# Kernel optimization log

Hardware: AMD Instinct MI355X
Metric: run time of the kernel (lower is better)

Reference implementation:

```python
import jax, jax.numpy as jnp
import numpy as np

B, S, D_IN, D_HID, D_OUT = 8, 2048, 1024, 1024, 1024


def setup_inputs() -> dict:
    key = jax.random.key(0)
    ks = jax.random.split(key, 11)
    def lin(kw, kb, fan_in, fan_out):
        bound = 1.0 / np.sqrt(fan_in)
        W = jax.random.uniform(kw, (fan_out, fan_in), minval=-bound, maxval=bound, dtype=jnp.float32)
        b = jax.random.uniform(kb, (fan_out,), minval=-bound, maxval=bound, dtype=jnp.float32)
        return W, b
    Wq, bq = lin(ks[0], ks[1], D_IN, D_HID)
    Wk, bk = lin(ks[2], ks[3], D_IN, D_HID)
    Wv, bv = lin(ks[4], ks[5], D_IN, D_HID)
    Wo, bo = lin(ks[6], ks[7], D_HID, D_OUT)
    gamma = jnp.ones((D_OUT,), jnp.float32)
    beta = jnp.zeros((D_OUT,), jnp.float32)
    x = jax.random.normal(ks[8], (B, S, D_IN), dtype=jnp.float32)
    return {"x": x, "Wq": Wq, "bq": bq, "Wk": Wk, "bk": bk,
            "Wv": Wv, "bv": bv, "Wo": Wo, "bo": bo,
            "gamma": gamma, "beta": beta}


def _layer_norm(x, gamma, beta, eps=1e-5):
    mu = jnp.mean(x, axis=-1, keepdims=True)
    var = jnp.var(x, axis=-1, keepdims=True)
    return (x - mu) * jax.lax.rsqrt(var + eps) * gamma + beta


def reference(x, Wq, bq, Wk, bk, Wv, bv, Wo, bo, gamma, beta):
    q = jnp.einsum('bsd,hd->bsh', x, Wq) + bq   # [B,S,H]
    k = jnp.einsum('bsd,hd->bsh', x, Wk) + bk
    v = jnp.einsum('bsd,hd->bsh', x, Wv) + bv
    scale = 1.0 / jnp.sqrt(jnp.float32(D_HID))
    scores = jnp.einsum('bqh,bkh->bqk', q, k) * scale  # [B,S,S]
    attn = jax.nn.softmax(scores, axis=-1)
    weighted = jnp.einsum('bqk,bkh->bqh', attn, v)     # [B,S,H]
    out = jnp.einsum('bsh,oh->bso', weighted, Wo) + bo # [B,S,O]
    return _layer_norm(out + x, gamma, beta)
```

## Files before the change

### kernel.cpp

```cpp
#include <hip/hip_runtime.h>
#include <hip/hip_bf16.h>
#include <math.h>


typedef __bf16 bf16;
typedef unsigned char u8;
typedef __attribute__((ext_vector_type(8))) __bf16 bf16x8;
typedef __attribute__((ext_vector_type(4))) __bf16 bf16x4;
typedef __attribute__((ext_vector_type(8))) int i32x8;
typedef __attribute__((ext_vector_type(16))) float f32x16;

__device__ __forceinline__ void async16(const u8* g, u8* l) {
    __builtin_amdgcn_global_load_lds(
        (const __attribute__((address_space(1))) void*)g,
        (__attribute__((address_space(3))) void*)l, 16, 0, 0);
}

#define WAITCNT_VM(n) __builtin_amdgcn_s_waitcnt((15 << 8) | (7 << 4) | (n))

__device__ __forceinline__ u8 to_fp8(float v) {
    return (u8)(__builtin_amdgcn_cvt_pk_fp8_f32(v, v, 0, 0) & 0xFF);
}

__global__ __launch_bounds__(256) void cast_f32_fp8(
    const float* __restrict__ in, u8* __restrict__ out, int n)
{
    int i = (blockIdx.x * 256 + threadIdx.x) * 8;
    if (i >= n) return;
    float4 a = *(const float4*)(in + i);
    float4 b = *(const float4*)(in + i + 4);
    int lo = __builtin_amdgcn_cvt_pk_fp8_f32(a.x, a.y, 0, 0);
    lo = __builtin_amdgcn_cvt_pk_fp8_f32(a.z, a.w, lo, 1);
    int hi = __builtin_amdgcn_cvt_pk_fp8_f32(b.x, b.y, 0, 0);
    hi = __builtin_amdgcn_cvt_pk_fp8_f32(b.z, b.w, hi, 1);
    int2 o = { lo, hi };
    *(int2*)(out + i) = o;
}

__global__ __launch_bounds__(256) void gemm_f8(
    const u8* __restrict__ A, long lda, long sA,
    const u8* __restrict__ B, long ldb, long sB,
    void* __restrict__ Cv, long ldc, long sC,
    const float* __restrict__ bias, int bias_mode,
    float scale, int c_mode, int K)
{
    __shared__ u8 lds[3][16384];

    const int gx = gridDim.x, gy = gridDim.y;
    const int slice = gx * gy;
    const int total = slice * gridDim.z;
    int flat = ((int)blockIdx.z * gy + (int)blockIdx.y) * gx + (int)blockIdx.x;
    if ((total & 7) == 0)
        flat = (flat & 7) * (total >> 3) + (flat >> 3);
    const int bz = flat / slice;
    const int rem = flat - bz * slice;
    const int by = rem / gx;
    const int bx = rem - by * gx;

    const int tid = threadIdx.x;
    const long tM = (long)by * 128;
    const long tN = (long)bx * 128;
    A += (long)bz * sA;
    B += (long)bz * sB;

    const int ra = tid >> 2;
    const int posc = tid & 3;
    const int ca = (posc ^ (ra & 3)) * 16;
    const u8* ga0 = A + (tM + ra) * lda + ca;
    const u8* ga1 = ga0 + 64 * lda;
    const u8* gb0 = B + (tN + ra) * ldb + ca;
    const u8* gb1 = gb0 + 64 * ldb;
    const int lo0 = tid * 16;
    const int lo1 = 4096 + tid * 16;
    const int lo2 = 8192 + tid * 16;
    const int lo3 = 12288 + tid * 16;

    const int w = tid >> 6, lane = tid & 63;
    const int wm = (w & 1) * 64, wn = (w >> 1) * 64;
    const int r32 = lane & 31, kh = lane >> 5;

    f32x16 acc[2][2] = {};

    const int iters = K >> 6;

    {
        u8* p0 = lds[0];
        async16(ga0, p0 + lo0); async16(ga1, p0 + lo1);
        async16(gb0, p0 + lo2); async16(gb1, p0 + lo3);
        u8* p1 = lds[1];
        async16(ga0 + 64, p1 + lo0); async16(ga1 + 64, p1 + lo1);
        async16(gb0 + 64, p1 + lo2); async16(gb1 + 64, p1 + lo3);
    }

    const int rowA0 = wm + r32, rowA1 = wm + 32 + r32;
    const int rowB0 = wn + r32, rowB1 = wn + 32 + r32;
    const int c0 = kh * 2, c1 = kh * 2 + 1;
    const int offA0q0 = rowA0 * 64 + ((c0 ^ (rowA0 & 3)) << 4);
    const int offA0q1 = rowA0 * 64 + ((c1 ^ (rowA0 & 3)) << 4);
    const int offA1q0 = rowA1 * 64 + ((c0 ^ (rowA1 & 3)) << 4);
    const int offA1q1 = rowA1 * 64 + ((c1 ^ (rowA1 & 3)) << 4);
    const int offB0q0 = 8192 + rowB0 * 64 + ((c0 ^ (rowB0 & 3)) << 4);
    const int offB0q1 = 8192 + rowB0 * 64 + ((c1 ^ (rowB0 & 3)) << 4);
    const int offB1q0 = 8192 + rowB1 * 64 + ((c0 ^ (rowB1 & 3)) << 4);
    const int offB1q1 = 8192 + rowB1 * 64 + ((c1 ^ (rowB1 & 3)) << 4);

    int cur = 0;
    for (int it = 0; it < iters; ++it) {
        if (it + 1 < iters) WAITCNT_VM(4);
        else WAITCNT_VM(0);
        __builtin_amdgcn_s_barrier();

        if (it + 2 < iters) {
            int nb = cur + 2; if (nb >= 3) nb -= 3;
            u8* p = lds[nb];
            const long ko = (long)(it + 2) << 6;
            async16(ga0 + ko, p + lo0); async16(ga1 + ko, p + lo1);
            async16(gb0 + ko, p + lo2); async16(gb1 + ko, p + lo3);
        }

        const u8* curb = lds[cur];
        union F { i32x8 v; int4 q[2]; };
        F a0, a1, b0, b1;
        a0.q[0] = *(const int4*)&curb[offA0q0];
        a0.q[1] = *(const int4*)&curb[offA0q1];
        a1.q[0] = *(const int4*)&curb[offA1q0];
        a1.q[1] = *(const int4*)&curb[offA1q1];
        b0.q[0] = *(const int4*)&curb[offB0q0];
        b0.q[1] = *(const int4*)&curb[offB0q1];
        b1.q[0] = *(const int4*)&curb[offB1q0];
        b1.q[1] = *(const int4*)&curb[offB1q1];

        acc[0][0] = __builtin_amdgcn_mfma_scale_f32_32x32x64_f8f6f4(
            a0.v, b0.v, acc[0][0], 0, 0, 0, 0x7F7F7F7F, 0, 0x7F7F7F7F);
        acc[0][1] = __builtin_amdgcn_mfma_scale_f32_32x32x64_f8f6f4(
            a0.v, b1.v, acc[0][1], 0, 0, 0, 0x7F7F7F7F, 0, 0x7F7F7F7F);
        acc[1][0] = __builtin_amdgcn_mfma_scale_f32_32x32x64_f8f6f4(
            a1.v, b0.v, acc[1][0], 0, 0, 0, 0x7F7F7F7F, 0, 0x7F7F7F7F);
        acc[1][1] = __builtin_amdgcn_mfma_scale_f32_32x32x64_f8f6f4(
            a1.v, b1.v, acc[1][1], 0, 0, 0, 0x7F7F7F7F, 0, 0x7F7F7F7F);

        if (++cur >= 3) cur = 0;
    }

#pragma unroll
    for (int i = 0; i < 2; i++) {
#pragma unroll
        for (int j = 0; j < 2; j++) {
            const long gn = tN + wn + j * 32 + r32;
            const float bn = (bias_mode == 1) ? bias[gn] : 0.0f;
#pragma unroll
            for (int reg = 0; reg < 16; reg++) {
                const int rowf = (reg & 3) + 8 * (reg >> 2) + 4 * kh;
                const long gm = tM + wm + i * 32 + rowf;
                float v = acc[i][j][reg] * scale + bn;
                if (bias_mode == 2) v += bias[gm];
                if (c_mode == 0)
                    ((bf16*)Cv + (long)bz * sC)[gm * ldc + gn] = (bf16)v;
                else
                    ((u8*)Cv + (long)bz * sC)[gm * ldc + gn] = to_fp8(v);
            }
        }
    }
}

__global__ __launch_bounds__(256) void softmax_f8(
    const bf16* __restrict__ S, u8* __restrict__ P)
{
    const long row = blockIdx.x;
    const bf16* p = S + row * 2048;
    const int t = threadIdx.x;

    bf16x8 v = *(const bf16x8*)(p + t * 8);
    float f[8];
    float m = -3.0e38f;
#pragma unroll
    for (int i = 0; i < 8; i++) { f[i] = (float)v[i]; m = fmaxf(m, f[i]); }
    for (int o = 32; o; o >>= 1) m = fmaxf(m, __shfl_down(m, o));

    __shared__ float sm[4], ssum[4];
    if ((t & 63) == 0) sm[t >> 6] = m;
    __syncthreads();
    m = fmaxf(fmaxf(sm[0], sm[1]), fmaxf(sm[2], sm[3]));

    float s = 0.0f;
#pragma unroll
    for (int i = 0; i < 8; i++) { f[i] = __expf(f[i] - m); s += f[i]; }
    for (int o = 32; o; o >>= 1) s += __shfl_down(s, o);
    if ((t & 63) == 0) ssum[t >> 6] = s;
    __syncthreads();
    s = ssum[0] + ssum[1] + ssum[2] + ssum[3];

    const float c = 256.0f / s;
    int lo = __builtin_amdgcn_cvt_pk_fp8_f32(f[0] * c, f[1] * c, 0, 0);
    lo = __builtin_amdgcn_cvt_pk_fp8_f32(f[2] * c, f[3] * c, lo, 1);
    int hi = __builtin_amdgcn_cvt_pk_fp8_f32(f[4] * c, f[5] * c, 0, 0);
    hi = __builtin_amdgcn_cvt_pk_fp8_f32(f[6] * c, f[7] * c, hi, 1);
    int2 o = { lo, hi };
    *(int2*)(P + row * 2048 + t * 8) = o;
}

__global__ __launch_bounds__(256) void ln_res(
    const bf16* __restrict__ pre, const float* __restrict__ x,
    const float* __restrict__ gamma, const float* __restrict__ beta,
    float* __restrict__ out)
{
    const long row = blockIdx.x;
    const int t = threadIdx.x;
    const long base = row * 1024 + t * 4;

    bf16x4 a = *(const bf16x4*)(pre + base);
    float4 b = *(const float4*)(x + base);
    float v0 = (float)a[0] + b.x, v1 = (float)a[1] + b.y;
    float v2 = (float)a[2] + b.z, v3 = (float)a[3] + b.w;

    float s = v0 + v1 + v2 + v3;
    float q = v0 * v0 + v1 * v1 + v2 * v2 + v3 * v3;
    for (int o = 32; o; o >>= 1) { s += __shfl_down(s, o); q += __shfl_down(q, o); }

    __shared__ float ls[4], lq[4];
    if ((t & 63) == 0) { ls[t >> 6] = s; lq[t >> 6] = q; }
    __syncthreads();
    s = ls[0] + ls[1] + ls[2] + ls[3];
    q = lq[0] + lq[1] + lq[2] + lq[3];

    const float mean = s * (1.0f / 1024.0f);
    const float var = q * (1.0f / 1024.0f) - mean * mean;
    const float rstd = rsqrtf(var + 1e-5f);

    const int c = t * 4;
    float4 g = *(const float4*)(gamma + c);
    float4 be = *(const float4*)(beta + c);
    float4 o;
    o.x = (v0 - mean) * rstd * g.x + be.x;
    o.y = (v1 - mean) * rstd * g.y + be.y;
    o.z = (v2 - mean) * rstd * g.z + be.z;
    o.w = (v3 - mean) * rstd * g.w + be.w;
    *(float4*)(out + base) = o;
}

extern "C" void kernel_launch(void* const* d_in, const int* in_sizes, int n_in,
                              void* d_out, int out_size, void* d_ws, size_t ws_size,
                              hipStream_t stream)
{
    const float* x     = (const float*)d_in[0];
    const float* Wq    = (const float*)d_in[1];
    const float* bq    = (const float*)d_in[2];
    const float* Wk    = (const float*)d_in[3];
    const float* bk    = (const float*)d_in[4];
    const float* Wv    = (const float*)d_in[5];
    const float* bv    = (const float*)d_in[6];
    const float* Wo    = (const float*)d_in[7];
    const float* bo    = (const float*)d_in[8];
    const float* gamma = (const float*)d_in[9];
    const float* beta  = (const float*)d_in[10];
    float* out = (float*)d_out;

    char* ws = (char*)d_ws;
    u8* x8  = (u8*)(ws + (size_t)0);
    u8* Q8  = (u8*)(ws + (size_t)16777216);
    u8* K8  = (u8*)(ws + (size_t)33554432);
    u8* VT8 = (u8*)(ws + (size_t)50331648);
    u8* P8  = (u8*)(ws + (size_t)67108864);
    bf16* Sb = (bf16*)(ws + (size_t)104857600);
    u8* Wq8 = (u8*)(ws + (size_t)176160768);
    u8* Wk8 = Wq8 + 1048576;
    u8* Wv8 = Wk8 + 1048576;
    u8* Wo8 = Wv8 + 1048576;

    cast_f32_fp8<<<8192, 256, 0, stream>>>(x, x8, 16777216);
    cast_f32_fp8<<<512, 256, 0, stream>>>(Wq, Wq8, 1048576);
    cast_f32_fp8<<<512, 256, 0, stream>>>(Wk, Wk8, 1048576);
    cast_f32_fp8<<<512, 256, 0, stream>>>(Wv, Wv8, 1048576);
    cast_f32_fp8<<<512, 256, 0, stream>>>(Wo, Wo8, 1048576);

    gemm_f8<<<dim3(8, 128, 1), 256, 0, stream>>>(
        x8, 1024, 0, Wq8, 1024, 0, (void*)Q8, 1024, 0, bq, 1, 1.0f, 1, 1024);
    gemm_f8<<<dim3(8, 128, 1), 256, 0, stream>>>(
        x8, 1024, 0, Wk8, 1024, 0, (void*)K8, 1024, 0, bk, 1, 1.0f, 1, 1024);
    gemm_f8<<<dim3(128, 8, 1), 256, 0, stream>>>(
        Wv8, 1024, 0, x8, 1024, 0, (void*)VT8, 16384, 0, bv, 2, 1.0f, 1, 1024);
    gemm_f8<<<dim3(16, 16, 8), 256, 0, stream>>>(
        Q8, 1024, 2097152, K8, 1024, 2097152, (void*)Sb, 2048, 4194304,
        nullptr, 0, 0.03125f, 0, 1024);
    softmax_f8<<<16384, 256, 0, stream>>>(Sb, P8);
    gemm_f8<<<dim3(8, 16, 8), 256, 0, stream>>>(
        P8, 2048, 4194304, VT8, 16384, 2048, (void*)Q8, 1024, 2097152,
        nullptr, 0, 0.0625f, 1, 2048);
    gemm_f8<<<dim3(8, 128, 1), 256, 0, stream>>>(
        Q8, 1024, 0, Wo8, 1024, 0, (void*)Sb, 1024, 0, bo, 1, 0.0625f, 0, 1024);
    ln_res<<<16384, 256, 0, stream>>>((const bf16*)Sb, x, gamma, beta, out);
}
```

Baseline: 454.3 us.

## Double the FP8 GEMM K-tile to 128 with double-buffered LDS

The FP8 MFMA GEMM now loads 128-wide K tiles into two 32 KB LDS buffers with an 8-chunk XOR swizzle, replacing the three-deep ring of 64-wide tiles. Each iteration issues 8 async loads and 8 MFMAs, which halves the number of barriers and loop iterations. In exchange, prefetch depth drops from two tiles ahead to one, and the loop waits for all outstanding loads (waitcnt 0) every iteration. LDS per block grows from 48 KB to 64 KB, which may reduce occupancy.

```diff
diff --git a/kernel.cpp b/kernel.cpp
--- a/kernel.cpp
+++ b/kernel.cpp
@@ -44,7 +44,7 @@
     const float* __restrict__ bias, int bias_mode,
     float scale, int c_mode, int K)
 {
-    __shared__ u8 lds[3][16384];
+    __shared__ u8 lds[2][32768];
 
     const int gx = gridDim.x, gy = gridDim.y;
     const int slice = gx * gy;
@@ -63,17 +63,11 @@
     A += (long)bz * sA;
     B += (long)bz * sB;
 
-    const int ra = tid >> 2;
-    const int posc = tid & 3;
-    const int ca = (posc ^ (ra & 3)) * 16;
-    const u8* ga0 = A + (tM + ra) * lda + ca;
-    const u8* ga1 = ga0 + 64 * lda;
-    const u8* gb0 = B + (tN + ra) * ldb + ca;
-    const u8* gb1 = gb0 + 64 * ldb;
-    const int lo0 = tid * 16;
-    const int lo1 = 4096 + tid * 16;
-    const int lo2 = 8192 + tid * 16;
-    const int lo3 = 12288 + tid * 16;
+    const int srow = tid >> 3;
+    const int schunk = (tid & 7) ^ (srow & 7);
+    const u8* gAs = A + (tM + srow) * lda + schunk * 16;
+    const u8* gBs = B + (tN + srow) * ldb + schunk * 16;
+    const int ldst = tid * 16;
 
     const int w = tid >> 6, lane = tid & 63;
     const int wm = (w & 1) * 64, wn = (w >> 1) * 64;
@@ -81,65 +75,86 @@
 
     f32x16 acc[2][2] = {};
 
-    const int iters = K >> 6;
+    const int iters = K >> 7;
 
     {
-        u8* p0 = lds[0];
-        async16(ga0, p0 + lo0); async16(ga1, p0 + lo1);
-        async16(gb0, p0 + lo2); async16(gb1, p0 + lo3);
-        u8* p1 = lds[1];
-        async16(ga0 + 64, p1 + lo0); async16(ga1 + 64, p1 + lo1);
-        async16(gb0 + 64, p1 + lo2); async16(gb1 + 64, p1 + lo3);
+        u8* p = lds[0];
+        async16(gAs,            p + ldst);
+        async16(gAs + 32 * lda, p + 4096 + ldst);
+        async16(gAs + 64 * lda, p + 8192 + ldst);
+        async16(gAs + 96 * lda, p + 12288 + ldst);
+        async16(gBs,            p + 16384 + ldst);
+        async16(gBs + 32 * ldb, p + 20480 + ldst);
+        async16(gBs + 64 * ldb, p + 24576 + ldst);
+        async16(gBs + 96 * ldb, p + 28672 + ldst);
     }
 
-    const int rowA0 = wm + r32, rowA1 = wm + 32 + r32;
-    const int rowB0 = wn + r32, rowB1 = wn + 32 + r32;
-    const int c0 = kh * 2, c1 = kh * 2 + 1;
-    const int offA0q0 = rowA0 * 64 + ((c0 ^ (rowA0 & 3)) << 4);
-    const int offA0q1 = rowA0 * 64 + ((c1 ^ (rowA0 & 3)) << 4);
-    const int offA1q0 = rowA1 * 64 + ((c0 ^ (rowA1 & 3)) << 4);
-    const int offA1q1 = rowA1 * 64 + ((c1 ^ (rowA1 & 3)) << 4);
-    const int offB0q0 = 8192 + rowB0 * 64 + ((c0 ^ (rowB0 & 3)) << 4);
-    const int offB0q1 = 8192 + rowB0 * 64 + ((c1 ^ (rowB0 & 3)) << 4);
-    const int offB1q0 = 8192 + rowB1 * 64 + ((c0 ^ (rowB1 & 3)) << 4);
-    const int offB1q1 = 8192 + rowB1 * 64 + ((c1 ^ (rowB1 & 3)) << 4);
+    const int xr = r32 & 7;
+    const int rA0 = (wm + r32) * 128;
+    const int rA1 = rA0 + 32 * 128;
+    const int rB0 = 16384 + (wn + r32) * 128;
+    const int rB1 = rB0 + 32 * 128;
+    const int c00 = (((kh << 1) + 0) ^ xr) << 4;
+    const int c01 = (((kh << 1) + 1) ^ xr) << 4;
+    const int c10 = ((4 + (kh << 1) + 0) ^ xr) << 4;
+    const int c11 = ((4 + (kh << 1) + 1) ^ xr) << 4;
 
     int cur = 0;
     for (int it = 0; it < iters; ++it) {
-        if (it + 1 < iters) WAITCNT_VM(4);
-        else WAITCNT_VM(0);
+        WAITCNT_VM(0);
         __builtin_amdgcn_s_barrier();
 
-        if (it + 2 < iters) {
-            int nb = cur + 2; if (nb >= 3) nb -= 3;
-            u8* p = lds[nb];
-            const long ko = (long)(it + 2) << 6;
-            async16(ga0 + ko, p + lo0); async16(ga1 + ko, p + lo1);
-            async16(gb0 + ko, p + lo2); async16(gb1 + ko, p + lo3);
+        if (it + 1 < iters) {
+            u8* p = lds[cur ^ 1];
+            const long ko = (long)(it + 1) << 7;
+            async16(gAs + ko,            p + ldst);
+            async16(gAs + 32 * lda + ko, p + 4096 + ldst);
+            async16(gAs + 64 * lda + ko, p + 8192 + ldst);
+            async16(gAs + 96 * lda + ko, p + 12288 + ldst);
+            async16(gBs + ko,            p + 16384 + ldst);
+            async16(gBs + 32 * ldb + ko, p + 20480 + ldst);
+            async16(gBs + 64 * ldb + ko, p + 24576 + ldst);
+            async16(gBs + 96 * ldb + ko, p + 28672 + ldst);
         }
 
         const u8* curb = lds[cur];
         union F { i32x8 v; int4 q[2]; };
-        F a0, a1, b0, b1;
-        a0.q[0] = *(const int4*)&curb[offA0q0];
-        a0.q[1] = *(const int4*)&curb[offA0q1];
-        a1.q[0] = *(const int4*)&curb[offA1q0];
-        a1.q[1] = *(const int4*)&curb[offA1q1];
-        b0.q[0] = *(const int4*)&curb[offB0q0];
-        b0.q[1] = *(const int4*)&curb[offB0q1];
-        b1.q[0] = *(const int4*)&curb[offB1q0];
-        b1.q[1] = *(const int4*)&curb[offB1q1];
+        F a0k0, a1k0, b0k0, b1k0, a0k1, a1k1, b0k1, b1k1;
+        a0k0.q[0] = *(const int4*)&curb[rA0 + c00];
+        a0k0.q[1] = *(const int4*)&curb[rA0 + c01];
+        a1k0.q[0] = *(const int4*)&curb[rA1 + c00];
+        a1k0.q[1] = *(const int4*)&curb[rA1 + c01];
+        b0k0.q[0] = *(const int4*)&curb[rB0 + c00];
+        b0k0.q[1] = *(const int4*)&curb[rB0 + c01];
+        b1k0.q[0] = *(const int4*)&curb[rB1 + c00];
+        b1k0.q[1] = *(const int4*)&curb[rB1 + c01];
+        a0k1.q[0] = *(const int4*)&curb[rA0 + c10];
+        a0k1.q[1] = *(const int4*)&curb[rA0 + c11];
+        a1k1.q[0] = *(const int4*)&curb[rA1 + c10];
+        a1k1.q[1] = *(const int4*)&curb[rA1 + c11];
+        b0k1.q[0] = *(const int4*)&curb[rB0 + c10];
+        b0k1.q[1] = *(const int4*)&curb[rB0 + c11];
+        b1k1.q[0] = *(const int4*)&curb[rB1 + c10];
+        b1k1.q[1] = *(const int4*)&curb[rB1 + c11];
 
         acc[0][0] = __builtin_amdgcn_mfma_scale_f32_32x32x64_f8f6f4(
-            a0.v, b0.v, acc[0][0], 0, 0, 0, 0x7F7F7F7F, 0, 0x7F7F7F7F);
+            a0k0.v, b0k0.v, acc[0][0], 0, 0, 0, 0x7F7F7F7F, 0, 0x7F7F7F7F);
         acc[0][1] = __builtin_amdgcn_mfma_scale_f32_32x32x64_f8f6f4(
-            a0.v, b1.v, acc[0][1], 0, 0, 0, 0x7F7F7F7F, 0, 0x7F7F7F7F);
+            a0k0.v, b1k0.v, acc[0][1], 0, 0, 0, 0x7F7F7F7F, 0, 0x7F7F7F7F);
         acc[1][0] = __builtin_amdgcn_mfma_scale_f32_32x32x64_f8f6f4(
-            a1.v, b0.v, acc[1][0], 0, 0, 0, 0x7F7F7F7F, 0, 0x7F7F7F7F);
+            a1k0.v, b0k0.v, acc[1][0], 0, 0, 0, 0x7F7F7F7F, 0, 0x7F7F7F7F);
         acc[1][1] = __builtin_amdgcn_mfma_scale_f32_32x32x64_f8f6f4(
-            a1.v, b1.v, acc[1][1], 0, 0, 0, 0x7F7F7F7F, 0, 0x7F7F7F7F);
-
-        if (++cur >= 3) cur = 0;
+            a1k0.v, b1k0.v, acc[1][1], 0, 0, 0, 0x7F7F7F7F, 0, 0x7F7F7F7F);
+        acc[0][0] = __builtin_amdgcn_mfma_scale_f32_32x32x64_f8f6f4(
+            a0k1.v, b0k1.v, acc[0][0], 0, 0, 0, 0x7F7F7F7F, 0, 0x7F7F7F7F);
+        acc[0][1] = __builtin_amdgcn_mfma_scale_f32_32x32x64_f8f6f4(
+            a0k1.v, b1k1.v, acc[0][1], 0, 0, 0, 0x7F7F7F7F, 0, 0x7F7F7F7F);
+        acc[1][0] = __builtin_amdgcn_mfma_scale_f32_32x32x64_f8f6f4(
+            a1k1.v, b0k1.v, acc[1][0], 0, 0, 0, 0x7F7F7F7F, 0, 0x7F7F7F7F);
+        acc[1][1] = __builtin_amdgcn_mfma_scale_f32_32x32x64_f8f6f4(
+            a1k1.v, b1k1.v, acc[1][1], 0, 0, 0, 0x7F7F7F7F, 0, 0x7F7F7F7F);
+
+        cur ^= 1;
     }
 
 #pragma unroll
```

New measurement: 408.2 us. 10.2% less time.

## Use 4-stage LDS ring with issue-before-barrier prefetch and new swizzle layout

Applied to the files above, without the earlier changes.

The fp8 GEMM now keeps four LDS stages instead of three, which lets the next prefetch be issued before the wait and barrier instead of after. The shared-memory tile layout changes to 128-byte lines with an 8-way XOR swizzle, simplifying the fragment offsets. MFMA sections are wrapped in s_setprio to favor matrix issue. The intent is better overlap of global loads with compute and fewer LDS bank conflicts, at the cost of 16KB more LDS per block, which may reduce occupancy.

```diff
diff --git a/kernel.cpp b/kernel.cpp
--- a/kernel.cpp
+++ b/kernel.cpp
@@ -44,7 +44,7 @@
     const float* __restrict__ bias, int bias_mode,
     float scale, int c_mode, int K)
 {
-    __shared__ u8 lds[3][16384];
+    __shared__ u8 lds[4][16384];
 
     const int gx = gridDim.x, gy = gridDim.y;
     const int slice = gx * gy;
@@ -63,17 +63,16 @@
     A += (long)bz * sA;
     B += (long)bz * sB;
 
-    const int ra = tid >> 2;
-    const int posc = tid & 3;
-    const int ca = (posc ^ (ra & 3)) * 16;
-    const u8* ga0 = A + (tM + ra) * lda + ca;
-    const u8* ga1 = ga0 + 64 * lda;
-    const u8* gb0 = B + (tN + ra) * ldb + ca;
-    const u8* gb1 = gb0 + 64 * ldb;
-    const int lo0 = tid * 16;
-    const int lo1 = 4096 + tid * 16;
-    const int lo2 = 8192 + tid * 16;
-    const int lo3 = 12288 + tid * 16;
+    const int sline = tid >> 3;
+    const int sch = (tid & 7) ^ (sline & 7);
+    const int skb = (sch & 3) << 4;
+    const int srofs = (sch & 4) << 4;
+    const u8* gA0 = A + (tM + sline + srofs) * lda + skb;
+    const u8* gA1 = gA0 + 32 * lda;
+    const u8* gB0 = B + (tN + sline + srofs) * ldb + skb;
+    const u8* gB1 = gB0 + 32 * ldb;
+    const int dA0 = tid * 16,        dA1 = 4096 + tid * 16;
+    const int dB0 = 8192 + tid * 16, dB1 = 12288 + tid * 16;
 
     const int w = tid >> 6, lane = tid & 63;
     const int wm = (w & 1) * 64, wn = (w >> 1) * 64;
@@ -84,52 +83,49 @@
     const int iters = K >> 6;
 
     {
-        u8* p0 = lds[0];
-        async16(ga0, p0 + lo0); async16(ga1, p0 + lo1);
-        async16(gb0, p0 + lo2); async16(gb1, p0 + lo3);
-        u8* p1 = lds[1];
-        async16(ga0 + 64, p1 + lo0); async16(ga1 + 64, p1 + lo1);
-        async16(gb0 + 64, p1 + lo2); async16(gb1 + 64, p1 + lo3);
+        u8* p = lds[0];
+        async16(gA0, p + dA0); async16(gA1, p + dA1);
+        async16(gB0, p + dB0); async16(gB1, p + dB1);
+        u8* q = lds[1];
+        async16(gA0 + 64, q + dA0); async16(gA1 + 64, q + dA1);
+        async16(gB0 + 64, q + dB0); async16(gB1 + 64, q + dB1);
     }
 
-    const int rowA0 = wm + r32, rowA1 = wm + 32 + r32;
-    const int rowB0 = wn + r32, rowB1 = wn + 32 + r32;
-    const int c0 = kh * 2, c1 = kh * 2 + 1;
-    const int offA0q0 = rowA0 * 64 + ((c0 ^ (rowA0 & 3)) << 4);
-    const int offA0q1 = rowA0 * 64 + ((c1 ^ (rowA0 & 3)) << 4);
-    const int offA1q0 = rowA1 * 64 + ((c0 ^ (rowA1 & 3)) << 4);
-    const int offA1q1 = rowA1 * 64 + ((c1 ^ (rowA1 & 3)) << 4);
-    const int offB0q0 = 8192 + rowB0 * 64 + ((c0 ^ (rowB0 & 3)) << 4);
-    const int offB0q1 = 8192 + rowB0 * 64 + ((c1 ^ (rowB0 & 3)) << 4);
-    const int offB1q0 = 8192 + rowB1 * 64 + ((c0 ^ (rowB1 & 3)) << 4);
-    const int offB1q1 = 8192 + rowB1 * 64 + ((c1 ^ (rowB1 & 3)) << 4);
-
-    int cur = 0;
+    const int xr = r32 & 7;
+    const int cbA = (w & 1) ? 4 : 0;
+    const int cbB = (w >> 1) ? 4 : 0;
+    const int oA0q0 = r32 * 128 + (((cbA + (kh << 1) + 0) ^ xr) << 4);
+    const int oA0q1 = r32 * 128 + (((cbA + (kh << 1) + 1) ^ xr) << 4);
+    const int oB0q0 = 8192 + r32 * 128 + (((cbB + (kh << 1) + 0) ^ xr) << 4);
+    const int oB0q1 = 8192 + r32 * 128 + (((cbB + (kh << 1) + 1) ^ xr) << 4);
+
     for (int it = 0; it < iters; ++it) {
-        if (it + 1 < iters) WAITCNT_VM(4);
-        else WAITCNT_VM(0);
+        if (it + 2 < iters) {
+            u8* p = lds[(it + 2) & 3];
+            const long ko = (long)(it + 2) << 6;
+            async16(gA0 + ko, p + dA0); async16(gA1 + ko, p + dA1);
+            async16(gB0 + ko, p + dB0); async16(gB1 + ko, p + dB1);
+            WAITCNT_VM(8);
+        } else if (it + 1 < iters) {
+            WAITCNT_VM(4);
+        } else {
+            WAITCNT_VM(0);
+        }
         __builtin_amdgcn_s_barrier();
 
-        if (it + 2 < iters) {
-            int nb = cur + 2; if (nb >= 3) nb -= 3;
-            u8* p = lds[nb];
-            const long ko = (long)(it + 2) << 6;
-            async16(ga0 + ko, p + lo0); async16(ga1 + ko, p + lo1);
-            async16(gb0 + ko, p + lo2); async16(gb1 + ko, p + lo3);
-        }
-
-        const u8* curb = lds[cur];
+        const u8* cb = lds[it & 3];
         union F { i32x8 v; int4 q[2]; };
         F a0, a1, b0, b1;
-        a0.q[0] = *(const int4*)&curb[offA0q0];
-        a0.q[1] = *(const int4*)&curb[offA0q1];
-        a1.q[0] = *(const int4*)&curb[offA1q0];
-        a1.q[1] = *(const int4*)&curb[offA1q1];
-        b0.q[0] = *(const int4*)&curb[offB0q0];
-        b0.q[1] = *(const int4*)&curb[offB0q1];
-        b1.q[0] = *(const int4*)&curb[offB1q0];
-        b1.q[1] = *(const int4*)&curb[offB1q1];
-
+        a0.q[0] = *(const int4*)&cb[oA0q0];
+        a0.q[1] = *(const int4*)&cb[oA0q1];
+        a1.q[0] = *(const int4*)&cb[oA0q0 + 4096];
+        a1.q[1] = *(const int4*)&cb[oA0q1 + 4096];
+        b0.q[0] = *(const int4*)&cb[oB0q0];
+        b0.q[1] = *(const int4*)&cb[oB0q1];
+        b1.q[0] = *(const int4*)&cb[oB0q0 + 4096];
+        b1.q[1] = *(const int4*)&cb[oB0q1 + 4096];
+
+        __builtin_amdgcn_s_setprio(1);
         acc[0][0] = __builtin_amdgcn_mfma_scale_f32_32x32x64_f8f6f4(
             a0.v, b0.v, acc[0][0], 0, 0, 0, 0x7F7F7F7F, 0, 0x7F7F7F7F);
         acc[0][1] = __builtin_amdgcn_mfma_scale_f32_32x32x64_f8f6f4(
@@ -138,8 +134,7 @@
             a1.v, b0.v, acc[1][0], 0, 0, 0, 0x7F7F7F7F, 0, 0x7F7F7F7F);
         acc[1][1] = __builtin_amdgcn_mfma_scale_f32_32x32x64_f8f6f4(
             a1.v, b1.v, acc[1][1], 0, 0, 0, 0x7F7F7F7F, 0, 0x7F7F7F7F);
-
-        if (++cur >= 3) cur = 0;
+        __builtin_amdgcn_s_setprio(0);
     }
 
 #pragma unroll
```

After: 434.6 us. 1.05x faster.
